# Kernel tuning notes

Measured on AMD Instinct MI355X. Metric: run time of the kernel, lower is better.

## Reference

```python
import jax, jax.numpy as jnp
import numpy as np

OUTPUT_SIZE = 16384          # number of map units (must be a perfect square)
SIDE = 128.0                 # sqrt(OUTPUT_SIZE)
SIGMA = 2.0                  # neighbourhood std-dev (non-trainable weight in original)
B, D = 2048, 256


def setup_inputs() -> dict:
    key = jax.random.key(0)
    k1, k2 = jax.random.split(key)
    x = jax.random.normal(k1, (B, D), dtype=jnp.float32)
    kernel = jax.random.normal(k2, (D, OUTPUT_SIZE), dtype=jnp.float32) * 0.1
    return {"x": x, "kernel": kernel}


def _grid_coords():
    # 2D coordinates of each flattened map unit: unit k -> (k // side, k % side)
    idx = jnp.arange(OUTPUT_SIZE, dtype=jnp.float32)
    return jnp.floor(idx / SIDE), jnp.mod(idx, SIDE)  # each (size,)


def reference(x, kernel):
    # Squared Euclidean distance of every sample to every prototype: (B, size).
    # Same math as tf.norm(x[:, :, None] - kernel[None])**2, expressed as a GEMM.
    norms2 = (jnp.sum(x * x, axis=1, keepdims=True)
              - 2.0 * (x @ kernel)
              + jnp.sum(kernel * kernel, axis=0, keepdims=True))
    norms2 = jnp.maximum(norms2, 0.0)

    # Winner-take-all unit per sample, mapped to 2D grid coordinates.
    wta = jnp.argmin(norms2, axis=1).astype(jnp.float32)        # (B,)
    mean_r = jnp.floor(wta / SIDE)                               # (B,)
    mean_c = jnp.mod(wta, SIDE)                                  # (B,)

    # Gaussian neighbourhood over the 2D grid, flattened: (B, size).
    gr, gc = _grid_coords()
    dr = gr[None, :] - mean_r[:, None]
    dc = gc[None, :] - mean_c[:, None]
    radials = jnp.exp(-0.5 / (SIGMA * SIGMA) * (dr * dr + dc * dc))

    return radials * norms2
```

## Files before the change

### kernel.cpp

```cpp
#include <hip/hip_runtime.h>
#include <hip/hip_fp16.h>

#define OUTN 16384
#define BATCH 2048
#define DIM   256

typedef _Float16 half8 __attribute__((ext_vector_type(8)));
typedef float    floatx4 __attribute__((ext_vector_type(4)));
typedef unsigned long long u64;

__device__ __forceinline__ void gl2lds16(const void* g, void* l) {
    __builtin_amdgcn_global_load_lds(
        (const __attribute__((address_space(1))) void*)g,
        (__attribute__((address_space(3))) void*)l, 16, 0, 0);
}

__device__ __forceinline__ u64 packkey(float v, int col) {
    unsigned u = __float_as_uint(v);
    u = (u & 0x80000000u) ? ~u : (u | 0x80000000u);
    return ((u64)u << 32) | (unsigned)col;
}
__device__ __forceinline__ float unpackval(u64 p) {
    unsigned u = (unsigned)(p >> 32);
    u = (u & 0x80000000u) ? (u & 0x7fffffffu) : ~u;
    return __uint_as_float(u);
}

__global__ __launch_bounds__(256) void prep_all(
        const float* __restrict__ x, const float* __restrict__ kern,
        _Float16* __restrict__ xh, float* __restrict__ rown,
        _Float16* __restrict__ kT, float* __restrict__ kT32,
        float* __restrict__ colnp) {
    int blk = blockIdx.x, t = threadIdx.x;
    if (blk < 512) {
        __shared__ float tile[64][65];
        __shared__ float npart[4][64];
        int tx = t & 63, ty = t >> 6;
        int j0 = (blk >> 1) * 64;
        int dhalf = blk & 1, dbase = dhalf * 128;
        float nrm = 0.f;
        for (int pc = 0; pc < 2; pc++) {
            int dc = dbase + pc * 64;
            __syncthreads();
            for (int it = 0; it < 16; it++) {
                int d = dc + ty + it * 4;
                float v = kern[(size_t)d * OUTN + j0 + tx];
                tile[ty + it * 4][tx] = v;
                nrm = fmaf(v, v, nrm);
            }
            __syncthreads();
            for (int c = t; c < 512; c += 256) {
                int j = c >> 3, o8 = (c & 7) * 8;
                half8 h; float vv[8];
                for (int u = 0; u < 8; u++) { vv[u] = tile[o8 + u][j]; h[u] = (_Float16)vv[u]; }
                *(half8*)&kT[(size_t)(j0 + j) * DIM + dc + o8] = h;
                float* kp = &kT32[(size_t)(j0 + j) * DIM + dc + o8];
                *(float4*)kp       = make_float4(vv[0], vv[1], vv[2], vv[3]);
                *(float4*)(kp + 4) = make_float4(vv[4], vv[5], vv[6], vv[7]);
            }
        }
        npart[ty][tx] = nrm;
        __syncthreads();
        if (t < 64)
            colnp[(size_t)dhalf * OUTN + j0 + t] =
                npart[0][t] + npart[1][t] + npart[2][t] + npart[3][t];
    } else {
        int b = blk - 512;
        float v = x[b * DIM + t];
        xh[b * DIM + t] = (_Float16)v;
        float s = v * v;
        for (int off = 32; off; off >>= 1) s += __shfl_down(s, off, 64);
        __shared__ float wsum[4];
        if ((t & 63) == 0) wsum[t >> 6] = s;
        __syncthreads();
        if (t == 0) rown[b] = wsum[0] + wsum[1] + wsum[2] + wsum[3];
    }
}

__global__ __launch_bounds__(256) void gemm_norms(
        const _Float16* __restrict__ xh, const _Float16* __restrict__ kT,
        const float* __restrict__ rown, const float* __restrict__ colnp,
        _Float16* __restrict__ n2h, u64* __restrict__ blockcand) {
    __shared__ __align__(16) char smem[35328];
    _Float16* As = (_Float16*)smem;
    _Float16* Bs = (_Float16*)(smem + 16384);
    u64* cand = (u64*)smem;
    _Float16* nb = (_Float16*)smem;
    float* rnl = (float*)(smem + 34816);
    int tid  = threadIdx.x;
    int col0 = blockIdx.x * 128;
    int row0 = blockIdx.y * 128;
    int wid = tid >> 6, lane = tid & 63;
    int wr = wid >> 1, wc = wid & 1;
    int l15 = lane & 15, l4 = lane >> 4;
    int xh7 = l15 & 7;

    if (tid < 128) rnl[tid] = rown[row0 + tid];

    floatx4 acc[4][4];
    for (int i = 0; i < 4; i++)
        for (int j = 0; j < 4; j++)
            acc[i][j] = (floatx4){0.f, 0.f, 0.f, 0.f};

    for (int kt = 0; kt < 4; kt++) {
        int k0 = kt * 64;
        for (int it = 0; it < 4; it++) {
            int chunk = it * 256 + tid;
            int r = chunk >> 3, gg = chunk & 7;
            int ksw = (gg ^ (r & 7)) * 8;
            gl2lds16(&xh[(size_t)(row0 + r) * DIM + k0 + ksw], &As[chunk * 8]);
            gl2lds16(&kT[(size_t)(col0 + r) * DIM + k0 + ksw], &Bs[chunk * 8]);
        }
        __syncthreads();
        for (int s = 0; s < 2; s++) {
            int g = s * 4 + l4;
            int sw = (g ^ xh7) * 8;
            half8 af[4], bf[4];
            for (int i = 0; i < 4; i++)
                af[i] = *(half8*)&As[(wr * 64 + i * 16 + l15) * 64 + sw];
            for (int j = 0; j < 4; j++)
                bf[j] = *(half8*)&Bs[(wc * 64 + j * 16 + l15) * 64 + sw];
            for (int i = 0; i < 4; i++)
                for (int j = 0; j < 4; j++)
                    acc[i][j] = __builtin_amdgcn_mfma_f32_16x16x32_f16(
                        af[i], bf[j], acc[i][j], 0, 0, 0);
        }
        __syncthreads();
    }

    float cn[4]; int oc[4];
    for (int j = 0; j < 4; j++) {
        oc[j] = col0 + wc * 64 + j * 16 + l15;
        cn[j] = colnp[oc[j]] + colnp[OUTN + oc[j]];
    }
    for (int i = 0; i < 4; i++) {
        for (int r = 0; r < 4; r++) {
            int row_l = wr * 64 + i * 16 + l4 * 4 + r;
            u64 best = ~0ull;
            for (int j = 0; j < 4; j++) {
                u64 pk = packkey(cn[j] - 2.0f * acc[i][j][r], oc[j]);
                if (pk < best) best = pk;
            }
            cand[row_l * 33 + wc * 16 + l15] = best;
        }
    }
    __syncthreads();
    if (tid < 128) {
        u64 m1 = ~0ull, m2 = ~0ull;
        for (int s = 0; s < 32; s++) {
            u64 v = cand[tid * 33 + s];
            if (v < m1) { m2 = m1; m1 = v; }
            else if (v < m2) { m2 = v; }
        }
        size_t base = (size_t)(row0 + tid) * 256 + blockIdx.x * 2;
        blockcand[base]     = m1;
        blockcand[base + 1] = m2;
    }
    __syncthreads();

    for (int i = 0; i < 4; i++) {
        for (int r = 0; r < 4; r++) {
            int row_l = wr * 64 + i * 16 + l4 * 4 + r;
            float rn = rnl[row_l];
            for (int j = 0; j < 4; j++)
                nb[row_l * 136 + wc * 64 + j * 16 + l15] =
                    (_Float16)(rn + cn[j] - 2.0f * acc[i][j][r]);
        }
    }
    __syncthreads();
    for (int c = tid; c < 2048; c += 256) {
        int r = c >> 4, o8 = (c & 15) * 8;
        *(half8*)&n2h[(size_t)(row0 + r) * OUTN + col0 + o8] =
            *(half8*)&nb[r * 136 + o8];
    }
}

__global__ __launch_bounds__(256) void refine_finalize(
        const u64* __restrict__ blockcand, const float* __restrict__ x,
        const float* __restrict__ kT32, const float* __restrict__ colnp,
        const _Float16* __restrict__ n2h, float* __restrict__ out) {
    int b = blockIdx.x, t = threadIdx.x;
    __shared__ float xrow[DIM];
    __shared__ u64 red[256];
    __shared__ float colf[128];
    xrow[t] = x[b * DIM + t];
    if (t < 128) colf[t] = __expf(-0.125f * (float)(t * t));
    u64 e = blockcand[(size_t)b * 256 + t];
    red[t] = e;
    __syncthreads();
    for (int off = 128; off; off >>= 1) {
        if (t < off) { u64 o = red[t + off]; if (o < red[t]) red[t] = o; }
        __syncthreads();
    }
    float minv = unpackval(red[0]);
    __syncthreads();

    u64 pk = ~0ull;
    if (unpackval(e) <= minv + 0.125f) {
        int j = (int)(e & 0xffffffffu);
        const float4* kr4 = (const float4*)(kT32 + (size_t)j * DIM);
        const float4* xr4 = (const float4*)xrow;
        float s0 = 0.f, s1 = 0.f, s2 = 0.f, s3 = 0.f;
        for (int q = 0; q < 64; q += 4) {
            float4 k0 = kr4[q],     x0 = xr4[q];
            float4 k1 = kr4[q + 1], x1 = xr4[q + 1];
            float4 k2 = kr4[q + 2], x2 = xr4[q + 2];
            float4 k3 = kr4[q + 3], x3 = xr4[q + 3];
            s0 = fmaf(k0.x, x0.x, fmaf(k0.y, x0.y, fmaf(k0.z, x0.z, fmaf(k0.w, x0.w, s0))));
            s1 = fmaf(k1.x, x1.x, fmaf(k1.y, x1.y, fmaf(k1.z, x1.z, fmaf(k1.w, x1.w, s1))));
            s2 = fmaf(k2.x, x2.x, fmaf(k2.y, x2.y, fmaf(k2.z, x2.z, fmaf(k2.w, x2.w, s2))));
            s3 = fmaf(k3.x, x3.x, fmaf(k3.y, x3.y, fmaf(k3.z, x3.z, fmaf(k3.w, x3.w, s3))));
        }
        float dot = (s0 + s1) + (s2 + s3);
        pk = packkey((colnp[j] + colnp[OUTN + j]) - 2.0f * dot, j);
    }
    red[t] = pk;
    __syncthreads();
    for (int off = 128; off; off >>= 1) {
        if (t < off) { u64 o = red[t + off]; if (o < red[t]) red[t] = o; }
        __syncthreads();
    }
    int w = (int)(red[0] & 0xffffffffu);
    int wrr = w >> 7, wcc = w & 127;

    const _Float16* nrow = n2h + (size_t)b * OUTN;
    float* orow = out + (size_t)b * OUTN;
    for (int c = t; c < 2048; c += 256) {
        int gr = c >> 4, o8 = (c & 15) * 8;
        int dr = gr - wrr; if (dr < 0) dr = -dr;
        float4 r0 = {0.f, 0.f, 0.f, 0.f}, r1 = {0.f, 0.f, 0.f, 0.f};
        if (dr <= 26) {
            float rowf = colf[dr];
            half8 h = *(const half8*)&nrow[gr * 128 + o8];
            float res[8];
            for (int u = 0; u < 8; u++) {
                int dc = o8 + u - wcc; if (dc < 0) dc = -dc;
                res[u] = rowf * colf[dc] * fmaxf((float)h[u], 0.f);
            }
            r0 = make_float4(res[0], res[1], res[2], res[3]);
            r1 = make_float4(res[4], res[5], res[6], res[7]);
        }
        *(float4*)&orow[gr * 128 + o8]     = r0;
        *(float4*)&orow[gr * 128 + o8 + 4] = r1;
    }
}

extern "C" void kernel_launch(void* const* d_in, const int* in_sizes, int n_in,
                              void* d_out, int out_size, void* d_ws, size_t ws_size,
                              hipStream_t stream) {
    const float* x    = (const float*)d_in[0];
    const float* kern = (const float*)d_in[1];
    float* out = (float*)d_out;
    char* ws = (char*)d_ws;

    _Float16* xh   = (_Float16*)(ws);
    _Float16* kT   = (_Float16*)(ws + (1u << 20));
    float*    kT32 = (float*)(ws + (9u << 20));
    float*   colnp = (float*)(ws + (25u << 20));
    float*    rown = (float*)(ws + (25u << 20) + (128u << 10));
    u64* blockcand = (u64*)(ws + (26u << 20));
    _Float16*  n2h = (_Float16*)(ws + (32u << 20));

    prep_all<<<2560, 256, 0, stream>>>(x, kern, xh, rown, kT, kT32, colnp);
    gemm_norms<<<dim3(OUTN / 128, BATCH / 128), 256, 0, stream>>>(
        xh, kT, rown, colnp, n2h, blockcand);
    refine_finalize<<<BATCH, 256, 0, stream>>>(blockcand, x, kT32, colnp, n2h, out);
}
```

Before: 204.9 us.

## Widen GEMM tile to 128x256 with 512 threads and skip distant columns in finalize

The GEMM block now covers 256 columns with 8 waves, so each loaded A tile is reused across twice as many columns. The epilogue runs the candidate reduction and fp16 staging in two halves so they fit the shared buffer. The finalize kernel now skips loading n2h chunks whose columns lie more than 26 from the winner, and zeroes any element beyond that distance. The tradeoffs are more LDS per block, extra barriers in the epilogue, and possibly lower occupancy.

```diff
diff --git a/kernel.cpp b/kernel.cpp
--- a/kernel.cpp
+++ b/kernel.cpp
@@ -77,21 +77,21 @@
     }
 }
 
-__global__ __launch_bounds__(256) void gemm_norms(
+__global__ __launch_bounds__(512, 4) void gemm_norms(
         const _Float16* __restrict__ xh, const _Float16* __restrict__ kT,
         const float* __restrict__ rown, const float* __restrict__ colnp,
         _Float16* __restrict__ n2h, u64* __restrict__ blockcand) {
-    __shared__ __align__(16) char smem[35328];
+    __shared__ __align__(16) char smem[49664];
     _Float16* As = (_Float16*)smem;
     _Float16* Bs = (_Float16*)(smem + 16384);
     u64* cand = (u64*)smem;
     _Float16* nb = (_Float16*)smem;
-    float* rnl = (float*)(smem + 34816);
+    float* rnl = (float*)(smem + 49152);
     int tid  = threadIdx.x;
-    int col0 = blockIdx.x * 128;
+    int col0 = blockIdx.x * 256;
     int row0 = blockIdx.y * 128;
     int wid = tid >> 6, lane = tid & 63;
-    int wr = wid >> 1, wc = wid & 1;
+    int wr = wid >> 2, wc = wid & 3;
     int l15 = lane & 15, l4 = lane >> 4;
     int xh7 = l15 & 7;
 
@@ -104,12 +104,18 @@
 
     for (int kt = 0; kt < 4; kt++) {
         int k0 = kt * 64;
-        for (int it = 0; it < 4; it++) {
-            int chunk = it * 256 + tid;
-            int r = chunk >> 3, gg = chunk & 7;
-            int ksw = (gg ^ (r & 7)) * 8;
-            gl2lds16(&xh[(size_t)(row0 + r) * DIM + k0 + ksw], &As[chunk * 8]);
-            gl2lds16(&kT[(size_t)(col0 + r) * DIM + k0 + ksw], &Bs[chunk * 8]);
+        for (int it = 0; it < 6; it++) {
+            int chunk = it * 512 + tid;
+            if (chunk < 1024) {
+                int r = chunk >> 3, gg = chunk & 7;
+                int ksw = (gg ^ (r & 7)) * 8;
+                gl2lds16(&xh[(size_t)(row0 + r) * DIM + k0 + ksw], &As[chunk * 8]);
+            } else {
+                int c2 = chunk - 1024;
+                int r = c2 >> 3, gg = c2 & 7;
+                int ksw = (gg ^ (r & 7)) * 8;
+                gl2lds16(&kT[(size_t)(col0 + r) * DIM + k0 + ksw], &Bs[c2 * 8]);
+            }
         }
         __syncthreads();
         for (int s = 0; s < 2; s++) {
@@ -133,45 +139,55 @@
         oc[j] = col0 + wc * 64 + j * 16 + l15;
         cn[j] = colnp[oc[j]] + colnp[OUTN + oc[j]];
     }
-    for (int i = 0; i < 4; i++) {
-        for (int r = 0; r < 4; r++) {
-            int row_l = wr * 64 + i * 16 + l4 * 4 + r;
-            u64 best = ~0ull;
-            for (int j = 0; j < 4; j++) {
-                u64 pk = packkey(cn[j] - 2.0f * acc[i][j][r], oc[j]);
-                if (pk < best) best = pk;
-            }
-            cand[row_l * 33 + wc * 16 + l15] = best;
-        }
-    }
-    __syncthreads();
-    if (tid < 128) {
-        u64 m1 = ~0ull, m2 = ~0ull;
-        for (int s = 0; s < 32; s++) {
-            u64 v = cand[tid * 33 + s];
-            if (v < m1) { m2 = m1; m1 = v; }
-            else if (v < m2) { m2 = v; }
-        }
-        size_t base = (size_t)(row0 + tid) * 256 + blockIdx.x * 2;
-        blockcand[base]     = m1;
-        blockcand[base + 1] = m2;
-    }
-    __syncthreads();
-
-    for (int i = 0; i < 4; i++) {
-        for (int r = 0; r < 4; r++) {
-            int row_l = wr * 64 + i * 16 + l4 * 4 + r;
-            float rn = rnl[row_l];
-            for (int j = 0; j < 4; j++)
-                nb[row_l * 136 + wc * 64 + j * 16 + l15] =
-                    (_Float16)(rn + cn[j] - 2.0f * acc[i][j][r]);
-        }
-    }
-    __syncthreads();
-    for (int c = tid; c < 2048; c += 256) {
-        int r = c >> 4, o8 = (c & 15) * 8;
-        *(half8*)&n2h[(size_t)(row0 + r) * OUTN + col0 + o8] =
-            *(half8*)&nb[r * 136 + o8];
+
+    for (int h = 0; h < 2; h++) {
+        __syncthreads();
+        if ((wc >> 1) == h) {
+            for (int i = 0; i < 4; i++) {
+                for (int r = 0; r < 4; r++) {
+                    int row_l = wr * 64 + i * 16 + l4 * 4 + r;
+                    u64 best = ~0ull;
+                    for (int j = 0; j < 4; j++) {
+                        u64 pk = packkey(cn[j] - 2.0f * acc[i][j][r], oc[j]);
+                        if (pk < best) best = pk;
+                    }
+                    cand[row_l * 33 + (wc & 1) * 16 + l15] = best;
+                }
+            }
+        }
+        __syncthreads();
+        if (tid < 128) {
+            u64 m1 = ~0ull, m2 = ~0ull;
+            for (int s = 0; s < 32; s++) {
+                u64 v = cand[tid * 33 + s];
+                if (v < m1) { m2 = m1; m1 = v; }
+                else if (v < m2) { m2 = v; }
+            }
+            size_t base = (size_t)(row0 + tid) * 256 + blockIdx.x * 4 + h * 2;
+            blockcand[base]     = m1;
+            blockcand[base + 1] = m2;
+        }
+    }
+
+    for (int h = 0; h < 2; h++) {
+        __syncthreads();
+        if ((wc >> 1) == h) {
+            for (int i = 0; i < 4; i++) {
+                for (int r = 0; r < 4; r++) {
+                    int row_l = wr * 64 + i * 16 + l4 * 4 + r;
+                    float rn = rnl[row_l];
+                    for (int j = 0; j < 4; j++)
+                        nb[row_l * 136 + (wc & 1) * 64 + j * 16 + l15] =
+                            (_Float16)(rn + cn[j] - 2.0f * acc[i][j][r]);
+                }
+            }
+        }
+        __syncthreads();
+        for (int c = tid; c < 2048; c += 512) {
+            int r = c >> 4, o8 = (c & 15) * 8;
+            *(half8*)&n2h[(size_t)(row0 + r) * OUTN + col0 + h * 128 + o8] =
+                *(half8*)&nb[r * 136 + o8];
+        }
     }
 }
 
@@ -229,13 +245,13 @@
         int gr = c >> 4, o8 = (c & 15) * 8;
         int dr = gr - wrr; if (dr < 0) dr = -dr;
         float4 r0 = {0.f, 0.f, 0.f, 0.f}, r1 = {0.f, 0.f, 0.f, 0.f};
-        if (dr <= 26) {
+        if (dr <= 26 && o8 + 7 >= wcc - 26 && o8 <= wcc + 26) {
             float rowf = colf[dr];
             half8 h = *(const half8*)&nrow[gr * 128 + o8];
             float res[8];
             for (int u = 0; u < 8; u++) {
                 int dc = o8 + u - wcc; if (dc < 0) dc = -dc;
-                res[u] = rowf * colf[dc] * fmaxf((float)h[u], 0.f);
+                res[u] = dc <= 26 ? rowf * colf[dc] * fmaxf((float)h[u], 0.f) : 0.f;
             }
             r0 = make_float4(res[0], res[1], res[2], res[3]);
             r1 = make_float4(res[4], res[5], res[6], res[7]);
@@ -262,7 +278,7 @@
     _Float16*  n2h = (_Float16*)(ws + (32u << 20));
 
     prep_all<<<2560, 256, 0, stream>>>(x, kern, xh, rown, kT, kT32, colnp);
-    gemm_norms<<<dim3(OUTN / 128, BATCH / 128), 256, 0, stream>>>(
+    gemm_norms<<<dim3(OUTN / 256, BATCH / 128), 512, 0, stream>>>(
         xh, kT, rown, colnp, n2h, blockcand);
     refine_finalize<<<BATCH, 256, 0, stream>>>(blockcand, x, kT32, colnp, n2h, out);
 }
```

Measured after the change: 213.4 us. +4.2%, slower.
